# Kernel tuning notes

Measured on AMD Instinct MI355X. Metric: run time of the kernel, lower is better.

Reference implementation:

```python
import jax, jax.numpy as jnp
import numpy as np

N = 50000
E = 800000
IN_F = 64
OUT_F = 64
EDGE_F = 16


def setup_inputs() -> dict:
    key = jax.random.key(0)
    ks = jax.random.split(key, 8)
    x = jax.random.normal(ks[0], (N, IN_F), dtype=jnp.float32)
    edge_index = jax.random.randint(ks[1], (2, E), 0, N, dtype=jnp.int64)
    edge_attr = jax.random.normal(ks[2], (E, EDGE_F), dtype=jnp.float32)
    # MLP params: Linear(2*IN_F+EDGE_F -> OUT_F), ReLU, Linear(OUT_F -> OUT_F)
    d_in = 2 * IN_F + EDGE_F
    s1 = 1.0 / np.sqrt(d_in)
    s2 = 1.0 / np.sqrt(OUT_F)
    W1 = jax.random.uniform(ks[3], (d_in, OUT_F), minval=-s1, maxval=s1, dtype=jnp.float32)
    b1 = jax.random.uniform(ks[4], (OUT_F,), minval=-s1, maxval=s1, dtype=jnp.float32)
    W2 = jax.random.uniform(ks[5], (OUT_F, OUT_F), minval=-s2, maxval=s2, dtype=jnp.float32)
    b2 = jax.random.uniform(ks[6], (OUT_F,), minval=-s2, maxval=s2, dtype=jnp.float32)
    return {"x": x, "edge_index": edge_index, "edge_attr": edge_attr,
            "W1": W1, "b1": b1, "W2": W2, "b2": b2}


def reference(x, edge_index, edge_attr, W1, b1, W2, b2):
    src, dst = edge_index[0], edge_index[1]
    # gather source/target node features, concat with edge features: (E, 2*IN_F+EDGE_F)
    msg_in = jnp.concatenate([x[src], x[dst], edge_attr], axis=-1)
    h = jax.nn.relu(msg_in @ W1 + b1)
    msg = h @ W2 + b2                      # (E, OUT_F)
    # scatter-sum messages to destination nodes: (N, OUT_F)
    out = jax.ops.segment_sum(msg, dst, num_segments=N)
    return out
```

## Files before the change

kernel.cpp:

```cpp
#include <hip/hip_runtime.h>

#define N_NODES 50000
#define N_EDGES 800000

typedef __attribute__((ext_vector_type(8))) short bf16x8;
typedef __attribute__((ext_vector_type(4))) float f32x4;

__device__ inline short f2bf(float f) {
    union { float f; unsigned u; } v; v.f = f;
    unsigned r = v.u + 0x7FFFu + ((v.u >> 16) & 1u);
    return (short)(r >> 16);
}

__global__ __launch_bounds__(256) void pre_kernel(
    const float* __restrict__ x, const float* __restrict__ W1,
    float* __restrict__ xa, float* __restrict__ xb)
{
    const int w = threadIdx.x >> 6;
    const int j = threadIdx.x & 63;
    const int gw = blockIdx.x * 4 + w;
    const int p = gw & 1;
    const int pair = gw >> 1;
    const int npair = (gridDim.x * 4) >> 1;

    float wc[64];
#pragma unroll
    for (int k = 0; k < 64; ++k) wc[k] = W1[(p * 64 + k) * 64 + j];

    float* __restrict__ outp = p ? xb : xa;

    for (int i = pair; i < N_NODES; i += npair) {
        const float4* xr = (const float4*)&x[(long)i * 64];
        float a0 = 0.f, a1 = 0.f, a2 = 0.f, a3 = 0.f;
#pragma unroll
        for (int k4 = 0; k4 < 16; ++k4) {
            float4 xv = xr[k4];
            a0 += xv.x * wc[k4 * 4 + 0];
            a1 += xv.y * wc[k4 * 4 + 1];
            a2 += xv.z * wc[k4 * 4 + 2];
            a3 += xv.w * wc[k4 * 4 + 3];
        }
        outp[(long)i * 64 + j] = (a0 + a1) + (a2 + a3);
    }
}

__global__ __launch_bounds__(256) void edge_mfma(
    const float* __restrict__ xa, const float* __restrict__ xb,
    const int* __restrict__ ei,
    const float* __restrict__ edge_attr,
    const float* __restrict__ W1, const float* __restrict__ b1,
    const float* __restrict__ W2, const float* __restrict__ b2,
    float* __restrict__ out)
{
    __shared__ __align__(16) unsigned short hbuf[4][16][72];

    const int w = threadIdx.x >> 6;
    const int l = threadIdx.x & 63;
    const int n = l & 15;
    const int q = l >> 4;

    bf16x8 w1f[4];
    bf16x8 w2f[4][2];
    float b1v[4], b2v[4];
#pragma unroll
    for (int t = 0; t < 4; ++t) {
        const int col = t * 16 + n;
#pragma unroll
        for (int i = 0; i < 8; ++i) {
            const int k = q * 8 + i;
            w1f[t][i] = (q < 2) ? f2bf(W1[(128 + k) * 64 + col]) : (short)0;
            w2f[t][0][i] = f2bf(W2[k * 64 + col]);
            w2f[t][1][i] = f2bf(W2[(32 + k) * 64 + col]);
        }
        b1v[t] = b1[col];
        b2v[t] = b2[col];
    }

    const int nwaves = gridDim.x * 4;
    const int gw = blockIdx.x * 4 + w;

    for (int tile = gw; tile < N_EDGES / 16; tile += nwaves) {
        const long eb = (long)tile * 16;

        int idxv = 0;
        if (l < 16)       idxv = ei[eb + l];
        else if (l < 32)  idxv = ei[(long)N_EDGES + eb + (l - 16)];

        int srcr[4], dstr[4];
#pragma unroll
        for (int r = 0; r < 4; ++r) {
            srcr[r] = __shfl(idxv, q * 4 + r);
            dstr[r] = __shfl(idxv, 16 + q * 4 + r);
        }

        bf16x8 eaf;
        if (q < 2) {
            const float* ep = &edge_attr[(eb + n) * 16 + q * 8];
            float4 e0 = *(const float4*)ep;
            float4 e1 = *(const float4*)(ep + 4);
            eaf[0] = f2bf(e0.x); eaf[1] = f2bf(e0.y);
            eaf[2] = f2bf(e0.z); eaf[3] = f2bf(e0.w);
            eaf[4] = f2bf(e1.x); eaf[5] = f2bf(e1.y);
            eaf[6] = f2bf(e1.z); eaf[7] = f2bf(e1.w);
        } else {
#pragma unroll
            for (int i = 0; i < 8; ++i) eaf[i] = (short)0;
        }

        f32x4 c1[4];
#pragma unroll
        for (int t = 0; t < 4; ++t) {
            f32x4 z = {0.f, 0.f, 0.f, 0.f};
            c1[t] = __builtin_amdgcn_mfma_f32_16x16x32_bf16(eaf, w1f[t], z, 0, 0, 0);
        }

        float g[4][4];
#pragma unroll
        for (int t = 0; t < 4; ++t)
#pragma unroll
            for (int r = 0; r < 4; ++r)
                g[t][r] = xa[(long)srcr[r] * 64 + t * 16 + n]
                        + xb[(long)dstr[r] * 64 + t * 16 + n];

#pragma unroll
        for (int t = 0; t < 4; ++t)
#pragma unroll
            for (int r = 0; r < 4; ++r) {
                float h = fmaxf(c1[t][r] + g[t][r] + b1v[t], 0.f);
                hbuf[w][q * 4 + r][t * 16 + n] = (unsigned short)f2bf(h);
            }

        bf16x8 hf0 = *(const bf16x8*)&hbuf[w][n][q * 8];
        bf16x8 hf1 = *(const bf16x8*)&hbuf[w][n][32 + q * 8];

        f32x4 c2[4];
#pragma unroll
        for (int t = 0; t < 4; ++t) {
            f32x4 z = {0.f, 0.f, 0.f, 0.f};
            c2[t] = __builtin_amdgcn_mfma_f32_16x16x32_bf16(hf0, w2f[t][0], z, 0, 0, 0);
            c2[t] = __builtin_amdgcn_mfma_f32_16x16x32_bf16(hf1, w2f[t][1], c2[t], 0, 0, 0);
        }

#pragma unroll
        for (int t = 0; t < 4; ++t)
#pragma unroll
            for (int r = 0; r < 4; ++r)
                unsafeAtomicAdd(&out[(long)dstr[r] * 64 + t * 16 + n],
                                c2[t][r] + b2v[t]);
    }
}

__global__ __launch_bounds__(256) void fallback_kernel(
    const float* __restrict__ x, const int* __restrict__ ei,
    const float* __restrict__ edge_attr,
    const float* __restrict__ W1, const float* __restrict__ b1,
    const float* __restrict__ W2, const float* __restrict__ b2,
    float* __restrict__ out)
{
    const int w = threadIdx.x >> 6;
    const int j = threadIdx.x & 63;
    const long e = (long)blockIdx.x * 4 + w;
    if (e >= N_EDGES) return;
    const int s  = ei[e];
    const int dd = ei[(long)N_EDGES + e];

    float acc = b1[j];
    for (int k = 0; k < 64; ++k) acc += x[(long)s  * 64 + k] * W1[k * 64 + j];
    for (int k = 0; k < 64; ++k) acc += x[(long)dd * 64 + k] * W1[(64 + k) * 64 + j];
    for (int k = 0; k < 16; ++k) acc += edge_attr[e * 16 + k] * W1[(128 + k) * 64 + j];
    const float h = fmaxf(acc, 0.f);

    float msg = b2[j];
    for (int k = 0; k < 64; ++k) msg += __shfl(h, k) * W2[k * 64 + j];
    unsafeAtomicAdd(&out[(long)dd * 64 + j], msg);
}

extern "C" void kernel_launch(void* const* d_in, const int* in_sizes, int n_in,
                              void* d_out, int out_size, void* d_ws, size_t ws_size,
                              hipStream_t stream) {
    const float* x   = (const float*)d_in[0];
    const int*   ei  = (const int*)d_in[1];
    const float* ea  = (const float*)d_in[2];
    const float* W1  = (const float*)d_in[3];
    const float* b1  = (const float*)d_in[4];
    const float* W2  = (const float*)d_in[5];
    const float* b2  = (const float*)d_in[6];
    float* out = (float*)d_out;

    hipMemsetAsync(out, 0, (size_t)N_NODES * 64 * sizeof(float), stream);

    const size_t need = (size_t)2 * N_NODES * 64 * sizeof(float);
    if (ws_size >= need) {
        float* xauf = (float*)d_ws;
        float* xbuf = xauf + (size_t)N_NODES * 64;
        pre_kernel<<<1024, 256, 0, stream>>>(x, W1, xauf, xbuf);
        edge_mfma<<<1024, 256, 0, stream>>>(xauf, xbuf, ei, ea,
                                            W1, b1, W2, b2, out);
    } else {
        fallback_kernel<<<N_EDGES / 4, 256, 0, stream>>>(x, ei, ea,
                                                         W1, b1, W2, b2, out);
    }
}
```

Baseline: 374.1 us.

## Sort edges by destination and pre-reduce messages before atomic scatter

Adds a counting sort of edges by destination (histogram, single-block scan, scatter into a permutation) and a new edge kernel that processes edges in sorted order. Within each 16-edge tile, messages are staged in shared memory and runs with the same destination are summed, so fewer global atomics are issued. Sorting also improves locality of xb gathers and output writes. In exchange it adds three extra launches, including a serial single-block scan, plus indirect loads through perm for indices and edge attributes.

```diff
diff --git a/kernel.cpp b/kernel.cpp
--- a/kernel.cpp
+++ b/kernel.cpp
@@ -41,6 +41,177 @@
             a3 += xv.w * wc[k4 * 4 + 3];
         }
         outp[(long)i * 64 + j] = (a0 + a1) + (a2 + a3);
+    }
+}
+
+__global__ __launch_bounds__(256) void hist_kernel(
+    const int* __restrict__ ei, int* __restrict__ cnt)
+{
+    const int e = blockIdx.x * 256 + threadIdx.x;
+    if (e < N_EDGES) atomicAdd(&cnt[ei[N_EDGES + e]], 1);
+}
+
+__global__ __launch_bounds__(1024) void scan_kernel(int* __restrict__ cnt)
+{
+    __shared__ int part[1024];
+    const int t = threadIdx.x;
+    const int base = t * 49;
+    int s = 0;
+#pragma unroll 7
+    for (int i = 0; i < 49; ++i) {
+        const int idx = base + i;
+        if (idx < N_NODES) s += cnt[idx];
+    }
+    part[t] = s;
+    __syncthreads();
+    for (int off = 1; off < 1024; off <<= 1) {
+        const int v = (t >= off) ? part[t - off] : 0;
+        __syncthreads();
+        part[t] += v;
+        __syncthreads();
+    }
+    int run = (t > 0) ? part[t - 1] : 0;
+    for (int i = 0; i < 49; ++i) {
+        const int idx = base + i;
+        if (idx < N_NODES) { const int c = cnt[idx]; cnt[idx] = run; run += c; }
+    }
+}
+
+__global__ __launch_bounds__(256) void scatter_kernel(
+    const int* __restrict__ ei, int* __restrict__ cur, int* __restrict__ perm)
+{
+    const int e = blockIdx.x * 256 + threadIdx.x;
+    if (e < N_EDGES) {
+        const int d = ei[N_EDGES + e];
+        const int p = atomicAdd(&cur[d], 1);
+        perm[p] = e;
+    }
+}
+
+__global__ __launch_bounds__(256) void edge_mfma_sorted(
+    const float* __restrict__ xa, const float* __restrict__ xb,
+    const int* __restrict__ ei, const int* __restrict__ perm,
+    const float* __restrict__ edge_attr,
+    const float* __restrict__ W1, const float* __restrict__ b1,
+    const float* __restrict__ W2, const float* __restrict__ b2,
+    float* __restrict__ out)
+{
+    __shared__ __align__(16) unsigned short hbuf[4][16][72];
+    __shared__ __align__(16) float msgbuf[4][16][68];
+    __shared__ int dstbuf[4][16];
+
+    const int w = threadIdx.x >> 6;
+    const int l = threadIdx.x & 63;
+    const int n = l & 15;
+    const int q = l >> 4;
+
+    bf16x8 w1f[4];
+    bf16x8 w2f[4][2];
+    float b1v[4], b2v[4];
+#pragma unroll
+    for (int t = 0; t < 4; ++t) {
+        const int col = t * 16 + n;
+#pragma unroll
+        for (int i = 0; i < 8; ++i) {
+            const int k = q * 8 + i;
+            w1f[t][i] = (q < 2) ? f2bf(W1[(128 + k) * 64 + col]) : (short)0;
+            w2f[t][0][i] = f2bf(W2[k * 64 + col]);
+            w2f[t][1][i] = f2bf(W2[(32 + k) * 64 + col]);
+        }
+        b1v[t] = b1[col];
+        b2v[t] = b2[col];
+    }
+
+    const int nwaves = gridDim.x * 4;
+    const int gw = blockIdx.x * 4 + w;
+
+    for (int tile = gw; tile < N_EDGES / 16; tile += nwaves) {
+        const long eb = (long)tile * 16;
+
+        const int pev = perm[eb + n];
+
+        int idxv = 0;
+        if (l < 16)       idxv = ei[pev];
+        else if (l < 32)  idxv = ei[(long)N_EDGES + pev];
+        if (l >= 16 && l < 32) dstbuf[w][l - 16] = idxv;
+
+        int srcr[4], dstr[4];
+#pragma unroll
+        for (int r = 0; r < 4; ++r) {
+            srcr[r] = __shfl(idxv, q * 4 + r);
+            dstr[r] = __shfl(idxv, 16 + q * 4 + r);
+        }
+
+        bf16x8 eaf;
+        if (q < 2) {
+            const float* ep = &edge_attr[(long)pev * 16 + q * 8];
+            float4 e0 = *(const float4*)ep;
+            float4 e1 = *(const float4*)(ep + 4);
+            eaf[0] = f2bf(e0.x); eaf[1] = f2bf(e0.y);
+            eaf[2] = f2bf(e0.z); eaf[3] = f2bf(e0.w);
+            eaf[4] = f2bf(e1.x); eaf[5] = f2bf(e1.y);
+            eaf[6] = f2bf(e1.z); eaf[7] = f2bf(e1.w);
+        } else {
+#pragma unroll
+            for (int i = 0; i < 8; ++i) eaf[i] = (short)0;
+        }
+
+        f32x4 c1[4];
+#pragma unroll
+        for (int t = 0; t < 4; ++t) {
+            f32x4 z = {0.f, 0.f, 0.f, 0.f};
+            c1[t] = __builtin_amdgcn_mfma_f32_16x16x32_bf16(eaf, w1f[t], z, 0, 0, 0);
+        }
+
+        float g[4][4];
+#pragma unroll
+        for (int t = 0; t < 4; ++t)
+#pragma unroll
+            for (int r = 0; r < 4; ++r)
+                g[t][r] = xa[(long)srcr[r] * 64 + t * 16 + n]
+                        + xb[(long)dstr[r] * 64 + t * 16 + n];
+
+#pragma unroll
+        for (int t = 0; t < 4; ++t)
+#pragma unroll
+            for (int r = 0; r < 4; ++r) {
+                const float h = fmaxf(c1[t][r] + g[t][r] + b1v[t], 0.f);
+                hbuf[w][q * 4 + r][t * 16 + n] = (unsigned short)f2bf(h);
+            }
+
+        bf16x8 hf0 = *(const bf16x8*)&hbuf[w][n][q * 8];
+        bf16x8 hf1 = *(const bf16x8*)&hbuf[w][n][32 + q * 8];
+
+        f32x4 c2[4];
+#pragma unroll
+        for (int t = 0; t < 4; ++t) {
+            f32x4 z = {0.f, 0.f, 0.f, 0.f};
+            c2[t] = __builtin_amdgcn_mfma_f32_16x16x32_bf16(hf0, w2f[t][0], z, 0, 0, 0);
+            c2[t] = __builtin_amdgcn_mfma_f32_16x16x32_bf16(hf1, w2f[t][1], c2[t], 0, 0, 0);
+        }
+
+#pragma unroll
+        for (int t = 0; t < 4; ++t)
+#pragma unroll
+            for (int r = 0; r < 4; ++r)
+                msgbuf[w][q * 4 + r][t * 16 + n] = c2[t][r] + b2v[t];
+
+        {
+            int cur = dstbuf[w][0];
+            float acc = msgbuf[w][0][l];
+#pragma unroll
+            for (int r16 = 1; r16 < 16; ++r16) {
+                const int d2 = dstbuf[w][r16];
+                const float v = msgbuf[w][r16][l];
+                if (d2 != cur) {
+                    unsafeAtomicAdd(&out[(long)cur * 64 + l], acc);
+                    cur = d2; acc = v;
+                } else {
+                    acc += v;
+                }
+            }
+            unsafeAtomicAdd(&out[(long)cur * 64 + l], acc);
+        }
     }
 }
 
@@ -81,7 +252,6 @@
 
     for (int tile = gw; tile < N_EDGES / 16; tile += nwaves) {
         const long eb = (long)tile * 16;
-
         int idxv = 0;
         if (l < 16)       idxv = ei[eb + l];
         else if (l < 32)  idxv = ei[(long)N_EDGES + eb + (l - 16)];
@@ -126,7 +296,7 @@
         for (int t = 0; t < 4; ++t)
 #pragma unroll
             for (int r = 0; r < 4; ++r) {
-                float h = fmaxf(c1[t][r] + g[t][r] + b1v[t], 0.f);
+                const float h = fmaxf(c1[t][r] + g[t][r] + b1v[t], 0.f);
                 hbuf[w][q * 4 + r][t * 16 + n] = (unsigned short)f2bf(h);
             }
 
@@ -189,8 +359,25 @@
 
     hipMemsetAsync(out, 0, (size_t)N_NODES * 64 * sizeof(float), stream);
 
-    const size_t need = (size_t)2 * N_NODES * 64 * sizeof(float);
-    if (ws_size >= need) {
+    const size_t need_base = (size_t)2 * N_NODES * 64 * sizeof(float);
+    const size_t need_full = need_base
+                           + (size_t)N_EDGES * sizeof(int)
+                           + (size_t)N_NODES * sizeof(int);
+
+    if (ws_size >= need_full) {
+        float* xauf = (float*)d_ws;
+        float* xbuf = xauf + (size_t)N_NODES * 64;
+        int*   perm = (int*)(xbuf + (size_t)N_NODES * 64);
+        int*   dcur = perm + N_EDGES;
+
+        hipMemsetAsync(dcur, 0, (size_t)N_NODES * sizeof(int), stream);
+        pre_kernel<<<1024, 256, 0, stream>>>(x, W1, xauf, xbuf);
+        hist_kernel<<<(N_EDGES + 255) / 256, 256, 0, stream>>>(ei, dcur);
+        scan_kernel<<<1, 1024, 0, stream>>>(dcur);
+        scatter_kernel<<<(N_EDGES + 255) / 256, 256, 0, stream>>>(ei, dcur, perm);
+        edge_mfma_sorted<<<1024, 256, 0, stream>>>(xauf, xbuf, ei, perm, ea,
+                                                   W1, b1, W2, b2, out);
+    } else if (ws_size >= need_base) {
         float* xauf = (float*)d_ws;
         float* xbuf = xauf + (size_t)N_NODES * 64;
         pre_kernel<<<1024, 256, 0, stream>>>(x, W1, xauf, xbuf);
```

Result: slower. 489.8 us (+30.9%).

## Sort edges by destination in a fused cooperative kernel and pre-reduce scatter atomics

Applied to the files above, without the earlier changes.

Adds a counting sort of edges by destination (histogram, grid-wide scan, scatter into a permutation), all inside one cooperative kernel with grid syncs. It also folds the output zeroing and node pre-projection into that kernel. The edge phase then walks the sorted order and sums runs of equal destinations within each 16-edge tile in shared memory before issuing atomics. The goal is fewer float atomics and fewer kernel launches, paid for with the sort passes, several grid barriers, and edge_attr reads that now follow the permutation instead of running contiguously.

```diff
diff --git a/kernel.cpp b/kernel.cpp
--- a/kernel.cpp
+++ b/kernel.cpp
@@ -1,7 +1,11 @@
 #include <hip/hip_runtime.h>
+#include <hip/hip_cooperative_groups.h>
+
+namespace cg = cooperative_groups;
 
 #define N_NODES 50000
 #define N_EDGES 800000
+#define NTILES  (N_EDGES / 16)
 
 typedef __attribute__((ext_vector_type(8))) short bf16x8;
 typedef __attribute__((ext_vector_type(4))) float f32x4;
@@ -12,16 +16,14 @@
     return (short)(r >> 16);
 }
 
-__global__ __launch_bounds__(256) void pre_kernel(
+__device__ __forceinline__ void pre_phase(
+    int gw, int nwaves, int j,
     const float* __restrict__ x, const float* __restrict__ W1,
     float* __restrict__ xa, float* __restrict__ xb)
 {
-    const int w = threadIdx.x >> 6;
-    const int j = threadIdx.x & 63;
-    const int gw = blockIdx.x * 4 + w;
     const int p = gw & 1;
     const int pair = gw >> 1;
-    const int npair = (gridDim.x * 4) >> 1;
+    const int npair = nwaves >> 1;
 
     float wc[64];
 #pragma unroll
@@ -44,18 +46,24 @@
     }
 }
 
-__global__ __launch_bounds__(256) void edge_mfma(
+union __align__(16) TileMem {
+    unsigned short h[16][72];
+    float          m[16][68];
+};
+
+__device__ __forceinline__ void edge_phase(
+    int gw, int nwaves, int w, int l,
     const float* __restrict__ xa, const float* __restrict__ xb,
-    const int* __restrict__ ei,
+    const int* __restrict__ perm, const int* __restrict__ ssrc,
+    const int* __restrict__ sdst,
     const float* __restrict__ edge_attr,
     const float* __restrict__ W1, const float* __restrict__ b1,
     const float* __restrict__ W2, const float* __restrict__ b2,
     float* __restrict__ out)
 {
-    __shared__ __align__(16) unsigned short hbuf[4][16][72];
-
-    const int w = threadIdx.x >> 6;
-    const int l = threadIdx.x & 63;
+    __shared__ TileMem tls[4];
+    __shared__ int dstbuf[4][16];
+
     const int n = l & 15;
     const int q = l >> 4;
 
@@ -76,26 +84,24 @@
         b2v[t] = b2[col];
     }
 
-    const int nwaves = gridDim.x * 4;
-    const int gw = blockIdx.x * 4 + w;
-
-    for (int tile = gw; tile < N_EDGES / 16; tile += nwaves) {
+    for (int tile = gw; tile < NTILES; tile += nwaves) {
         const long eb = (long)tile * 16;
 
-        int idxv = 0;
-        if (l < 16)       idxv = ei[eb + l];
-        else if (l < 32)  idxv = ei[(long)N_EDGES + eb + (l - 16)];
+        const int pev = perm[eb + n];
+        const int sv  = ssrc[eb + n];
+        const int dv  = sdst[eb + n];
+        if (l < 16) dstbuf[w][n] = dv;
 
         int srcr[4], dstr[4];
 #pragma unroll
         for (int r = 0; r < 4; ++r) {
-            srcr[r] = __shfl(idxv, q * 4 + r);
-            dstr[r] = __shfl(idxv, 16 + q * 4 + r);
+            srcr[r] = __shfl(sv, q * 4 + r);
+            dstr[r] = __shfl(dv, q * 4 + r);
         }
 
         bf16x8 eaf;
         if (q < 2) {
-            const float* ep = &edge_attr[(eb + n) * 16 + q * 8];
+            const float* ep = &edge_attr[(long)pev * 16 + q * 8];
             float4 e0 = *(const float4*)ep;
             float4 e1 = *(const float4*)(ep + 4);
             eaf[0] = f2bf(e0.x); eaf[1] = f2bf(e0.y);
@@ -126,12 +132,12 @@
         for (int t = 0; t < 4; ++t)
 #pragma unroll
             for (int r = 0; r < 4; ++r) {
-                float h = fmaxf(c1[t][r] + g[t][r] + b1v[t], 0.f);
-                hbuf[w][q * 4 + r][t * 16 + n] = (unsigned short)f2bf(h);
+                const float h = fmaxf(c1[t][r] + g[t][r] + b1v[t], 0.f);
+                tls[w].h[q * 4 + r][t * 16 + n] = (unsigned short)f2bf(h);
             }
 
-        bf16x8 hf0 = *(const bf16x8*)&hbuf[w][n][q * 8];
-        bf16x8 hf1 = *(const bf16x8*)&hbuf[w][n][32 + q * 8];
+        bf16x8 hf0 = *(const bf16x8*)&tls[w].h[n][q * 8];
+        bf16x8 hf1 = *(const bf16x8*)&tls[w].h[n][32 + q * 8];
 
         f32x4 c2[4];
 #pragma unroll
@@ -145,9 +151,182 @@
         for (int t = 0; t < 4; ++t)
 #pragma unroll
             for (int r = 0; r < 4; ++r)
-                unsafeAtomicAdd(&out[(long)dstr[r] * 64 + t * 16 + n],
-                                c2[t][r] + b2v[t]);
-    }
+                tls[w].m[q * 4 + r][t * 16 + n] = c2[t][r] + b2v[t];
+
+        {
+            int cur = dstbuf[w][0];
+            float acc = tls[w].m[0][l];
+#pragma unroll
+            for (int r16 = 1; r16 < 16; ++r16) {
+                const int d2 = dstbuf[w][r16];
+                const float v = tls[w].m[r16][l];
+                if (d2 != cur) {
+                    unsafeAtomicAdd(&out[(long)cur * 64 + l], acc);
+                    cur = d2; acc = v;
+                } else {
+                    acc += v;
+                }
+            }
+            unsafeAtomicAdd(&out[(long)cur * 64 + l], acc);
+        }
+    }
+}
+
+__global__ __launch_bounds__(256, 4) void fused_kernel(
+    const float* __restrict__ x, const int* __restrict__ ei,
+    const float* __restrict__ ea,
+    const float* __restrict__ W1, const float* __restrict__ b1,
+    const float* __restrict__ W2, const float* __restrict__ b2,
+    float* __restrict__ out,
+    float* __restrict__ xa, float* __restrict__ xb,
+    int* __restrict__ perm, int* __restrict__ ssrc, int* __restrict__ sdst,
+    int* __restrict__ cnt, int* __restrict__ partials)
+{
+    cg::grid_group grid = cg::this_grid();
+    __shared__ int sscan[256];
+
+    const int tid = blockIdx.x * 256 + threadIdx.x;
+    const int nthreads = gridDim.x * 256;
+    const int w = threadIdx.x >> 6;
+    const int l = threadIdx.x & 63;
+    const int gw = blockIdx.x * 4 + w;
+    const int nwaves = gridDim.x * 4;
+
+    for (int i = tid; i < N_NODES * 16; i += nthreads) {
+        float4 z = {0.f, 0.f, 0.f, 0.f};
+        ((float4*)out)[i] = z;
+    }
+    for (int i = tid; i < N_NODES; i += nthreads) cnt[i] = 0;
+    pre_phase(gw, nwaves, l, x, W1, xa, xb);
+    __threadfence(); grid.sync(); __threadfence();
+
+    for (int e = tid; e < N_EDGES; e += nthreads)
+        atomicAdd(&cnt[ei[N_EDGES + e]], 1);
+    __threadfence(); grid.sync(); __threadfence();
+
+    const int v = (tid < N_NODES) ? cnt[tid] : 0;
+    sscan[threadIdx.x] = v;
+    __syncthreads();
+    for (int off = 1; off < 256; off <<= 1) {
+        const int t = (threadIdx.x >= off) ? sscan[threadIdx.x - off] : 0;
+        __syncthreads();
+        sscan[threadIdx.x] += t;
+        __syncthreads();
+    }
+    const int incl = sscan[threadIdx.x];
+    const int excl = incl - v;
+    if (threadIdx.x == 255) partials[blockIdx.x] = incl;
+    __threadfence(); grid.sync(); __threadfence();
+
+    if (blockIdx.x == 0) {
+        const int G = gridDim.x;
+        const int per = (G + 255) / 256;
+        int loc[8];
+        int s = 0;
+#pragma unroll
+        for (int i2 = 0; i2 < 8; ++i2) {
+            const int idx = threadIdx.x * per + i2;
+            const int c = (i2 < per && idx < G) ? partials[idx] : 0;
+            loc[i2] = s; s += c;
+        }
+        sscan[threadIdx.x] = s;
+        __syncthreads();
+        for (int off = 1; off < 256; off <<= 1) {
+            const int t = (threadIdx.x >= off) ? sscan[threadIdx.x - off] : 0;
+            __syncthreads();
+            sscan[threadIdx.x] += t;
+            __syncthreads();
+        }
+        const int ex = sscan[threadIdx.x] - s;
+#pragma unroll
+        for (int i2 = 0; i2 < 8; ++i2) {
+            const int idx = threadIdx.x * per + i2;
+            if (i2 < per && idx < G) partials[idx] = ex + loc[i2];
+        }
+    }
+    __threadfence(); grid.sync(); __threadfence();
+
+    if (tid < N_NODES) atomicExch(&cnt[tid], excl + partials[blockIdx.x]);
+    __threadfence(); grid.sync(); __threadfence();
+
+    for (int e = tid; e < N_EDGES; e += nthreads) {
+        const int d = ei[N_EDGES + e];
+        const int s = ei[e];
+        const int p = atomicAdd(&cnt[d], 1);
+        perm[p] = e; ssrc[p] = s; sdst[p] = d;
+    }
+    __threadfence(); grid.sync(); __threadfence();
+
+    edge_phase(gw, nwaves, w, l, xa, xb, perm, ssrc, sdst,
+               ea, W1, b1, W2, b2, out);
+}
+
+__global__ __launch_bounds__(256) void pre_kernel(
+    const float* __restrict__ x, const float* __restrict__ W1,
+    float* __restrict__ xa, float* __restrict__ xb)
+{
+    pre_phase(blockIdx.x * 4 + (threadIdx.x >> 6), gridDim.x * 4,
+              threadIdx.x & 63, x, W1, xa, xb);
+}
+
+__global__ __launch_bounds__(256) void hist_kernel(
+    const int* __restrict__ ei, int* __restrict__ cnt)
+{
+    const int e = blockIdx.x * 256 + threadIdx.x;
+    if (e < N_EDGES) atomicAdd(&cnt[ei[N_EDGES + e]], 1);
+}
+
+__global__ __launch_bounds__(1024) void scan_kernel(int* __restrict__ cnt)
+{
+    __shared__ int part[1024];
+    const int t = threadIdx.x;
+    const int base = t * 49;
+    int s = 0;
+#pragma unroll 7
+    for (int i = 0; i < 49; ++i) {
+        const int idx = base + i;
+        if (idx < N_NODES) s += cnt[idx];
+    }
+    part[t] = s;
+    __syncthreads();
+    for (int off = 1; off < 1024; off <<= 1) {
+        const int v = (t >= off) ? part[t - off] : 0;
+        __syncthreads();
+        part[t] += v;
+        __syncthreads();
+    }
+    int run = (t > 0) ? part[t - 1] : 0;
+    for (int i = 0; i < 49; ++i) {
+        const int idx = base + i;
+        if (idx < N_NODES) { const int c = cnt[idx]; cnt[idx] = run; run += c; }
+    }
+}
+
+__global__ __launch_bounds__(256) void scatter_kernel(
+    const int* __restrict__ ei, int* __restrict__ cur,
+    int* __restrict__ perm, int* __restrict__ ssrc, int* __restrict__ sdst)
+{
+    const int e = blockIdx.x * 256 + threadIdx.x;
+    if (e < N_EDGES) {
+        const int d = ei[N_EDGES + e];
+        const int s = ei[e];
+        const int p = atomicAdd(&cur[d], 1);
+        perm[p] = e; ssrc[p] = s; sdst[p] = d;
+    }
+}
+
+__global__ __launch_bounds__(256) void edge_sorted_kernel(
+    const float* __restrict__ xa, const float* __restrict__ xb,
+    const int* __restrict__ perm, const int* __restrict__ ssrc,
+    const int* __restrict__ sdst,
+    const float* __restrict__ ea,
+    const float* __restrict__ W1, const float* __restrict__ b1,
+    const float* __restrict__ W2, const float* __restrict__ b2,
+    float* __restrict__ out)
+{
+    edge_phase(blockIdx.x * 4 + (threadIdx.x >> 6), gridDim.x * 4,
+               threadIdx.x >> 6, threadIdx.x & 63,
+               xa, xb, perm, ssrc, sdst, ea, W1, b1, W2, b2, out);
 }
 
 __global__ __launch_bounds__(256) void fallback_kernel(
@@ -187,16 +366,42 @@
     const float* b2  = (const float*)d_in[6];
     float* out = (float*)d_out;
 
-    hipMemsetAsync(out, 0, (size_t)N_NODES * 64 * sizeof(float), stream);
-
-    const size_t need = (size_t)2 * N_NODES * 64 * sizeof(float);
-    if (ws_size >= need) {
-        float* xauf = (float*)d_ws;
-        float* xbuf = xauf + (size_t)N_NODES * 64;
-        pre_kernel<<<1024, 256, 0, stream>>>(x, W1, xauf, xbuf);
-        edge_mfma<<<1024, 256, 0, stream>>>(xauf, xbuf, ei, ea,
-                                            W1, b1, W2, b2, out);
+    float* xa   = (float*)d_ws;
+    float* xb   = xa + (size_t)N_NODES * 64;
+    int* perm   = (int*)(xb + (size_t)N_NODES * 64);
+    int* ssrc   = perm + N_EDGES;
+    int* sdst   = ssrc + N_EDGES;
+    int* cnt    = sdst + N_EDGES;
+    int* parts  = cnt + N_NODES;
+    const size_t need_full = (size_t)((char*)(parts + 2048) - (char*)d_ws);
+    const size_t need_base = (size_t)2 * N_NODES * 64 * sizeof(float);
+
+    if (ws_size >= need_full) {
+        int nb = 0;
+        hipError_t oe = hipOccupancyMaxActiveBlocksPerMultiprocessor(
+            &nb, (const void*)fused_kernel, 256, 0);
+        int G = (oe == hipSuccess && nb > 0) ? nb * 256 : 512;
+        if (G > 1280) G = 1280;
+        if (G < 256)  G = 256;
+
+        void* args[] = { (void*)&x, (void*)&ei, (void*)&ea, (void*)&W1,
+                         (void*)&b1, (void*)&W2, (void*)&b2, (void*)&out,
+                         (void*)&xa, (void*)&xb, (void*)&perm, (void*)&ssrc,
+                         (void*)&sdst, (void*)&cnt, (void*)&parts };
+        hipError_t err = hipLaunchCooperativeKernel(
+            (const void*)fused_kernel, dim3(G), dim3(256), args, 0, stream);
+        if (err == hipSuccess) return;
+
+        hipMemsetAsync(out, 0, (size_t)N_NODES * 64 * sizeof(float), stream);
+        hipMemsetAsync(cnt, 0, (size_t)N_NODES * sizeof(int), stream);
+        pre_kernel<<<1024, 256, 0, stream>>>(x, W1, xa, xb);
+        hist_kernel<<<(N_EDGES + 255) / 256, 256, 0, stream>>>(ei, cnt);
+        scan_kernel<<<1, 1024, 0, stream>>>(cnt);
+        scatter_kernel<<<(N_EDGES + 255) / 256, 256, 0, stream>>>(ei, cnt, perm, ssrc, sdst);
+        edge_sorted_kernel<<<1024, 256, 0, stream>>>(xa, xb, perm, ssrc, sdst,
+                                                     ea, W1, b1, W2, b2, out);
     } else {
+        hipMemsetAsync(out, 0, (size_t)N_NODES * 64 * sizeof(float), stream);
         fallback_kernel<<<N_EDGES / 4, 256, 0, stream>>>(x, ei, ea,
                                                          W1, b1, W2, b2, out);
     }
```

After: 1.343 ms. +258.9%, slower.
